# Kernel optimization log

Hardware: AMD Instinct MI355X
Metric: run time of the kernel (lower is better)

## Reference

```python
import jax, jax.numpy as jnp
import numpy as np

NEG_SLOPE = 0.2


def _gat_conv(x, src, dst, W, a_src, a_dst, b, n_nodes):
    # Single-head PyG GATConv (normalize arg in source is ignored by GATConv).
    h = x @ W                                   # [N, C_out]
    e_src = h @ a_src                           # [N] alpha_src contribution
    e_dst = h @ a_dst                           # [N] alpha_dst contribution
    logits = jax.nn.leaky_relu(e_src[src] + e_dst[dst], NEG_SLOPE)  # [E]
    m = jax.ops.segment_max(logits, dst, num_segments=n_nodes)      # per-dst max
    e = jnp.exp(logits - m[dst])
    denom = jax.ops.segment_sum(e, dst, num_segments=n_nodes)
    alpha = e / denom[dst]                      # edge softmax over in-neighbors
    out = jax.ops.segment_sum(h[src] * alpha[:, None], dst, num_segments=n_nodes)
    return out + b


def _add_self_loops(edge_index, n_nodes):
    loop = jnp.arange(n_nodes, dtype=edge_index.dtype)
    src = jnp.concatenate([edge_index[0], loop])
    dst = jnp.concatenate([edge_index[1], loop])
    return src, dst


def setup_inputs() -> dict:
    key = jax.random.key(0)
    ks = jax.random.split(key, 16)
    N, E, C_IN, C_HID, C_OUT = 50000, 1600000, 128, 128, 64
    x = jax.random.normal(ks[0], (N, C_IN), dtype=jnp.float32)
    edge_index = jax.random.randint(ks[1], (2, E), 0, N, dtype=jnp.int32)
    glorot = lambda k, shape: jax.random.normal(k, shape, jnp.float32) * np.sqrt(2.0 / sum(shape))
    return {
        "x": x,
        "edge_index": edge_index,
        "W0": glorot(ks[2], (C_IN, C_HID)),
        "as0": glorot(ks[3], (C_HID,)) * 0.1,
        "ad0": glorot(ks[4], (C_HID,)) * 0.1,
        "b0": jnp.zeros((C_HID,), jnp.float32),
        "W1": glorot(ks[5], (C_HID, C_HID)),
        "as1": glorot(ks[6], (C_HID,)) * 0.1,
        "ad1": glorot(ks[7], (C_HID,)) * 0.1,
        "b1": jnp.zeros((C_HID,), jnp.float32),
        "W2": glorot(ks[8], (C_HID, C_OUT)),
        "as2": glorot(ks[9], (C_OUT,)) * 0.1,
        "ad2": glorot(ks[10], (C_OUT,)) * 0.1,
        "b2": jnp.zeros((C_OUT,), jnp.float32),
    }


def reference(x, edge_index, W0, as0, ad0, b0, W1, as1, ad1, b1, W2, as2, ad2, b2):
    n_nodes = x.shape[0]
    src, dst = _add_self_loops(edge_index, n_nodes)
    # eval mode: F.dropout with training=False is identity
    h = jax.nn.relu(_gat_conv(x, src, dst, W0, as0, ad0, b0, n_nodes))
    h = jax.nn.relu(_gat_conv(h, src, dst, W1, as1, ad1, b1, n_nodes))
    out = _gat_conv(h, src, dst, W2, as2, ad2, b2, n_nodes)
    return out
```

## Files before the change

kernel.cpp:

```cpp
#include <hip/hip_runtime.h>
#include <hip/hip_bf16.h>
#include <type_traits>

#define DEVFN __device__ __forceinline__

typedef __attribute__((ext_vector_type(8))) short bfrag;
typedef __attribute__((ext_vector_type(4))) float facc4;
typedef __attribute__((ext_vector_type(2))) float f32x2;

DEVFN float lrelu(float v) { return (v >= 0.f) ? v : 0.2f * v; }

DEVFN float bf_lo(unsigned u) { return __uint_as_float(u << 16); }
DEVFN float bf_hi(unsigned u) { return __uint_as_float(u & 0xFFFF0000u); }
DEVFN f32x2 upk2(unsigned u) {
  f32x2 r; r.x = bf_lo(u); r.y = bf_hi(u); return r;
}
DEVFN unsigned short f2bf(float f) {
  __hip_bfloat16 h = __float2bfloat16(f);
  return *reinterpret_cast<unsigned short*>(&h);
}
DEVFN unsigned packbf2(float x, float y) {
  return (unsigned)f2bf(x) | ((unsigned)f2bf(y) << 16);
}

DEVFN float wave_sum(float v) {
#pragma unroll
  for (int o = 1; o < 64; o <<= 1) v += __shfl_xor(v, o, 64);
  return v;
}
DEVFN float wave_max(float v) {
#pragma unroll
  for (int o = 1; o < 64; o <<= 1) v = fmaxf(v, __shfl_xor(v, o, 64));
  return v;
}

#define FMA_ROW(p_, v_)                                                  \
  {                                                                      \
    f32x2 pv; pv.x = (p_); pv.y = (p_);                                  \
    acc2[0] += pv * upk2((v_).x);                                        \
    acc2[1] += pv * upk2((v_).y);                                        \
    acc2[2] += pv * upk2((v_).z);                                        \
    acc2[3] += pv * upk2((v_).w);                                        \
  }

template<int C, bool A_FP32>
__global__ __launch_bounds__(256) void gemm_mfma(const void* __restrict__ Xin,
                                                 const float* __restrict__ W,
                                                 const float* __restrict__ a_src,
                                                 const float* __restrict__ a_dst,
                                                 unsigned short* __restrict__ H,
                                                 float* __restrict__ es,
                                                 float* __restrict__ ed,
                                                 int N) {
  constexpr int K = 128;
  constexpr int LSTR = K + 8;
  constexpr int NT = C / 16;
  __shared__ unsigned short WsT[C * LSTR];

  const int t = threadIdx.x;
  for (int i = t; i < K * C; i += 256) {
    int k = i / C;
    int c = i - k * C;
    WsT[c * LSTR + k] = f2bf(W[i]);
  }
  __syncthreads();

  const int wave = t >> 6;
  const int lane = t & 63;
  const int l15 = lane & 15;
  const int quad = lane >> 4;
  const int arow = blockIdx.x * 64 + wave * 16 + l15;
  const bool avalid = arow < N;

  facc4 acc[NT];
#pragma unroll
  for (int i = 0; i < NT; ++i) acc[i] = (facc4){0.f, 0.f, 0.f, 0.f};

#pragma unroll
  for (int ks = 0; ks < 4; ++ks) {
    bfrag a;
    if (A_FP32) {
      if (avalid) {
        const float* xp = (const float*)Xin + (size_t)arow * K + quad * 8 + ks * 32;
        float4 u = *(const float4*)xp;
        float4 v = *(const float4*)(xp + 4);
        a[0] = (short)f2bf(u.x); a[1] = (short)f2bf(u.y);
        a[2] = (short)f2bf(u.z); a[3] = (short)f2bf(u.w);
        a[4] = (short)f2bf(v.x); a[5] = (short)f2bf(v.y);
        a[6] = (short)f2bf(v.z); a[7] = (short)f2bf(v.w);
      } else {
        a = (bfrag){0, 0, 0, 0, 0, 0, 0, 0};
      }
    } else {
      const unsigned short* xp =
          (const unsigned short*)Xin + (size_t)arow * K + quad * 8 + ks * 32;
      a = *(const bfrag*)xp;
    }
#pragma unroll
    for (int ct = 0; ct < NT; ++ct) {
      bfrag b = *(const bfrag*)(&WsT[(ct * 16 + l15) * LSTR + ks * 32 + quad * 8]);
      acc[ct] = __builtin_amdgcn_mfma_f32_16x16x32_bf16(a, b, acc[ct], 0, 0, 0);
    }
  }

  float asv[NT], adv[NT];
#pragma unroll
  for (int ct = 0; ct < NT; ++ct) {
    asv[ct] = a_src[ct * 16 + l15];
    adv[ct] = a_dst[ct * 16 + l15];
  }

  const int orow0 = blockIdx.x * 64 + wave * 16 + quad * 4;
#pragma unroll
  for (int r = 0; r < 4; ++r) {
    const int orow = orow0 + r;
    float ps = 0.f, pd = 0.f;
#pragma unroll
    for (int ct = 0; ct < NT; ++ct) {
      if (orow < N) H[(size_t)orow * C + ct * 16 + l15] = f2bf(acc[ct][r]);
      ps += acc[ct][r] * asv[ct];
      pd += acc[ct][r] * adv[ct];
    }
#pragma unroll
    for (int msk = 1; msk < 16; msk <<= 1) {
      ps += __shfl_xor(ps, msk, 64);
      pd += __shfl_xor(pd, msk, 64);
    }
    if (l15 == 0 && orow < N) { es[orow] = ps; ed[orow] = pd; }
  }
}

__global__ void hist_only(const int* __restrict__ dst, int* __restrict__ hmat,
                          int E, int nbk, int chunk) {
  __shared__ int hist[4 * 128];
  const int t = threadIdx.x;
  for (int i = t; i < 4 * 128; i += 256) hist[i] = 0;
  __syncthreads();
  int* h = &hist[(t >> 6) << 7];
  const int e0 = blockIdx.x * chunk;
  const int e1 = min(E, e0 + chunk);
  for (int e = e0 + t; e < e1; e += 256) {
    atomicAdd(&h[dst[e] >> 9], 1);
  }
  __syncthreads();
  if (t < nbk)
    hmat[t * gridDim.x + blockIdx.x] =
        hist[t] + hist[t + 128] + hist[t + 256] + hist[t + 384];
}

__global__ void scan_partial(const int* __restrict__ in, int* __restrict__ csum, int n) {
  __shared__ int sh[256];
  int i = blockIdx.x * 256 + threadIdx.x;
  sh[threadIdx.x] = (i < n) ? in[i] : 0;
  __syncthreads();
  for (int o = 128; o > 0; o >>= 1) {
    if (threadIdx.x < o) sh[threadIdx.x] += sh[threadIdx.x + o];
    __syncthreads();
  }
  if (threadIdx.x == 0) csum[blockIdx.x] = sh[0];
}

__global__ void scan_chunks(int* __restrict__ csum, int nch) {
  __shared__ int sh[256];
  __shared__ int carry;
  if (threadIdx.x == 0) carry = 0;
  __syncthreads();
  for (int base = 0; base < nch; base += 256) {
    int i = base + threadIdx.x;
    int v = (i < nch) ? csum[i] : 0;
    sh[threadIdx.x] = v;
    __syncthreads();
    for (int o = 1; o < 256; o <<= 1) {
      int t = (threadIdx.x >= o) ? sh[threadIdx.x - o] : 0;
      __syncthreads();
      sh[threadIdx.x] += t;
      __syncthreads();
    }
    if (i < nch) csum[i] = carry + sh[threadIdx.x] - v;
    __syncthreads();
    if (threadIdx.x == 255) carry += sh[255];
    __syncthreads();
  }
}

__global__ void scan_final(const int* __restrict__ deg, const int* __restrict__ csum,
                           int* __restrict__ rp, int* __restrict__ wp, int N, int E) {
  __shared__ int sh[256];
  int i = blockIdx.x * 256 + threadIdx.x;
  int v = (i < N) ? deg[i] : 0;
  sh[threadIdx.x] = v;
  __syncthreads();
  for (int o = 1; o < 256; o <<= 1) {
    int t = (threadIdx.x >= o) ? sh[threadIdx.x - o] : 0;
    __syncthreads();
    sh[threadIdx.x] += t;
    __syncthreads();
  }
  if (i < N) {
    int r = csum[blockIdx.x] + sh[threadIdx.x] - v;
    rp[i] = r;
    wp[i] = r;
  }
  if (blockIdx.x == 0 && threadIdx.x == 0) rp[N] = E;
}

__global__ void scan_final_excl(const int* __restrict__ in, const int* __restrict__ csum,
                                int* __restrict__ out, int n) {
  __shared__ int sh[256];
  int i = blockIdx.x * 256 + threadIdx.x;
  int v = (i < n) ? in[i] : 0;
  sh[threadIdx.x] = v;
  __syncthreads();
  for (int o = 1; o < 256; o <<= 1) {
    int t = (threadIdx.x >= o) ? sh[threadIdx.x - o] : 0;
    __syncthreads();
    sh[threadIdx.x] += t;
    __syncthreads();
  }
  if (i < n) out[i] = csum[blockIdx.x] + sh[threadIdx.x] - v;
}

__global__ void place_pass(const int* __restrict__ src, const int* __restrict__ dst,
                           const int* __restrict__ off, unsigned* __restrict__ be,
                           int E, int nbk, int chunk) {
  __shared__ int cur[128];
  const int t = threadIdx.x;
  if (t < nbk) cur[t] = off[t * gridDim.x + blockIdx.x];
  __syncthreads();
  const int e0 = blockIdx.x * chunk;
  const int e1 = min(E, e0 + chunk);
  for (int e = e0 + t; e < e1; e += 256) {
    int d = dst[e];
    int s = src[e];
    int p = atomicAdd(&cur[d >> 9], 1);
    be[p] = (unsigned)s | ((unsigned)d << 16);
  }
}

__global__ void bucket_final(const unsigned* __restrict__ be, const int* __restrict__ off,
                             int* __restrict__ rp, unsigned short* __restrict__ col,
                             int E, int N, int nbk, int pblk) {
  __shared__ int cur[512];
  __shared__ int ps[256];
  const int b = blockIdx.x;
  const int n0 = b << 9;
  const int cnt = min(512, N - n0);
  const int t = threadIdx.x;
  for (int i = t; i < cnt; i += 256) cur[i] = 0;
  __syncthreads();
  const int e0 = off[b * pblk];
  const int e1 = (b + 1 < nbk) ? off[(b + 1) * pblk] : E;
  for (int e = e0 + t; e < e1; e += 256) {
    unsigned sd = be[e];
    atomicAdd(&cur[(int)(sd >> 16) - n0], 1);
  }
  __syncthreads();
  const int i0 = 2 * t, i1 = 2 * t + 1;
  const int v0 = (i0 < cnt) ? cur[i0] : 0;
  const int v1 = (i1 < cnt) ? cur[i1] : 0;
  ps[t] = v0 + v1;
  __syncthreads();
  for (int o = 1; o < 256; o <<= 1) {
    int u = (t >= o) ? ps[t - o] : 0;
    __syncthreads();
    ps[t] += u;
    __syncthreads();
  }
  const int base = e0 + ps[t] - (v0 + v1);
  if (i0 < cnt) { rp[n0 + i0] = base;      cur[i0] = base; }
  if (i1 < cnt) { rp[n0 + i1] = base + v0; cur[i1] = base + v0; }
  if (b == nbk - 1 && t == 0) rp[N] = E;
  __syncthreads();
  for (int e = e0 + t; e < e1; e += 256) {
    unsigned sd = be[e];
    int p = atomicAdd(&cur[(int)(sd >> 16) - n0], 1);
    col[p] = (unsigned short)(sd & 0xFFFFu);
  }
}

__global__ void csr_scatter_ranged(const int* __restrict__ src,
                                   const int* __restrict__ dst,
                                   int* __restrict__ wp, int* __restrict__ col,
                                   int E, int range, int npass) {
  const int stride = gridDim.x * blockDim.x;
  const int gid = blockIdx.x * blockDim.x + threadIdx.x;
  for (int pass = 0; pass < npass; ++pass) {
    const int lo = pass * range;
    const int hi = lo + range;
    for (int e = gid; e < E; e += stride) {
      int d = dst[e];
      if (d >= lo && d < hi) {
        int p = atomicAdd(wp + d, 1);
        col[p] = src[e];
      }
    }
  }
}

__global__ void csr_count(const int* __restrict__ dst, int* __restrict__ deg, int E) {
  int e = blockIdx.x * blockDim.x + threadIdx.x;
  if (e < E) atomicAdd(deg + dst[e], 1);
}

template<bool RELU, typename IT>
__global__ void gat_fused128(const int* __restrict__ row_ptr,
                             const IT* __restrict__ col,
                             const float* __restrict__ es,
                             const float* __restrict__ ed,
                             const unsigned short* __restrict__ H,
                             const float* __restrict__ bias,
                             void* __restrict__ outX, int N) {
  const int lane = threadIdx.x & 63;
  const int n = blockIdx.x * (blockDim.x >> 6) + (threadIdx.x >> 6);
  if (n >= N) return;

  const int g4 = lane >> 4;
  const int l15 = lane & 15;

  const int k0 = row_ptr[n];
  const int k1 = row_ptr[n + 1];
  const int deg = k1 - k0;
  const float edd = ed[n];
  const float self_lg = lrelu(es[n] + edd);

  const char* Hb = (const char*)H;
  f32x2 acc2[4];
#pragma unroll
  for (int i = 0; i < 4; ++i) { acc2[i].x = 0.f; acc2[i].y = 0.f; }
  float den, sp;

  if (deg <= 64) {
    int k = k0 + lane;
    bool act = (k < k1);
    int c = act ? (int)col[k] : 0;
    float lg = act ? lrelu(es[c] + edd) : -3.0e38f;
    float m = fmaxf(wave_max(lg), self_lg);
    float p = act ? __expf(lg - m) : 0.f;
    sp = __expf(self_lg - m);
    den = wave_sum(p) + sp;

    if (deg > 0) {
      int i0 = g4;
      int i1 = min(4 + g4, 63);
      int c0 = __shfl(c, i0);
      int c1 = __shfl(c, i1);
      uint4 v0 = *(const uint4*)(Hb + (((size_t)c0 << 8) + l15 * 16));
      uint4 v1 = *(const uint4*)(Hb + (((size_t)c1 << 8) + l15 * 16));
      const int nb = (deg + 7) >> 3;
      for (int t = 0; t + 1 < nb; ++t) {
        int ni0 = min(8 * t + 8 + g4, 63);
        int ni1 = min(8 * t + 12 + g4, 63);
        int nc0 = __shfl(c, ni0);
        int nc1 = __shfl(c, ni1);
        uint4 u0 = *(const uint4*)(Hb + (((size_t)nc0 << 8) + l15 * 16));
        uint4 u1 = *(const uint4*)(Hb + (((size_t)nc1 << 8) + l15 * 16));
        float p0 = __shfl(p, i0);
        float p1 = __shfl(p, i1);
        FMA_ROW(p0, v0);
        FMA_ROW(p1, v1);
        v0 = u0; v1 = u1; i0 = ni0; i1 = ni1;
      }
      float p0 = __shfl(p, i0);
      float p1 = __shfl(p, i1);
      FMA_ROW(p0, v0);
      FMA_ROW(p1, v1);
    }
  } else {
    float mloc = self_lg;
    for (int base = k0; base < k1; base += 64) {
      int k = base + lane;
      if (k < k1) mloc = fmaxf(mloc, lrelu(es[(int)col[k]] + edd));
    }
    float m = wave_max(mloc);
    sp = __expf(self_lg - m);
    den = sp;
    for (int base = k0; base < k1; base += 64) {
      int k = base + lane;
      bool act = (k < k1);
      int c = act ? (int)col[k] : 0;
      float p = act ? __expf(lrelu(es[c] + edd) - m) : 0.f;
      den += wave_sum(p);
      int len = min(64, k1 - base);
      for (int j = 0; j < len; j += 8) {
        int i0 = min(j + g4, 63);
        int i1 = min(j + 4 + g4, 63);
        int c0 = __shfl(c, i0);
        int c1 = __shfl(c, i1);
        float p0 = __shfl(p, i0);
        float p1 = __shfl(p, i1);
        uint4 v0 = *(const uint4*)(Hb + (((size_t)c0 << 8) + l15 * 16));
        uint4 v1 = *(const uint4*)(Hb + (((size_t)c1 << 8) + l15 * 16));
        FMA_ROW(p0, v0);
        FMA_ROW(p1, v1);
      }
    }
  }

  float a[8];
#pragma unroll
  for (int i = 0; i < 4; ++i) { a[2 * i] = acc2[i].x; a[2 * i + 1] = acc2[i].y; }
#pragma unroll
  for (int i = 0; i < 8; ++i) {
    a[i] += __shfl_xor(a[i], 16, 64);
    a[i] += __shfl_xor(a[i], 32, 64);
  }

  uint4 hv = *(const uint4*)(Hb + (((size_t)n << 8) + l15 * 16));
  a[0] += sp * bf_lo(hv.x); a[1] += sp * bf_hi(hv.x);
  a[2] += sp * bf_lo(hv.y); a[3] += sp * bf_hi(hv.y);
  a[4] += sp * bf_lo(hv.z); a[5] += sp * bf_hi(hv.z);
  a[6] += sp * bf_lo(hv.w); a[7] += sp * bf_hi(hv.w);

  float inv = 1.f / den;
  float4 bv0 = *(const float4*)(bias + l15 * 8);
  float4 bv1 = *(const float4*)(bias + l15 * 8 + 4);
  float o0 = a[0] * inv + bv0.x, o1 = a[1] * inv + bv0.y;
  float o2 = a[2] * inv + bv0.z, o3 = a[3] * inv + bv0.w;
  float o4 = a[4] * inv + bv1.x, o5 = a[5] * inv + bv1.y;
  float o6 = a[6] * inv + bv1.z, o7 = a[7] * inv + bv1.w;
  if (RELU) {
    o0 = fmaxf(o0, 0.f); o1 = fmaxf(o1, 0.f); o2 = fmaxf(o2, 0.f);
    o3 = fmaxf(o3, 0.f); o4 = fmaxf(o4, 0.f); o5 = fmaxf(o5, 0.f);
    o6 = fmaxf(o6, 0.f); o7 = fmaxf(o7, 0.f);
  }
  if (g4 == 0) {
    uint4 w;
    w.x = packbf2(o0, o1); w.y = packbf2(o2, o3);
    w.z = packbf2(o4, o5); w.w = packbf2(o6, o7);
    *(uint4*)((char*)outX + (((size_t)n << 8) + l15 * 16)) = w;
  }
}

template<bool RELU, typename IT>
__global__ void gat_fused64(const int* __restrict__ row_ptr,
                            const IT* __restrict__ col,
                            const float* __restrict__ es,
                            const float* __restrict__ ed,
                            const unsigned short* __restrict__ H,
                            const float* __restrict__ bias,
                            float* __restrict__ outX, int N) {
  const int lane = threadIdx.x & 63;
  const int n = blockIdx.x * (blockDim.x >> 6) + (threadIdx.x >> 6);
  if (n >= N) return;

  const int g8 = lane >> 3;
  const int l8 = lane & 7;

  const int k0 = row_ptr[n];
  const int k1 = row_ptr[n + 1];
  const int deg = k1 - k0;
  const float edd = ed[n];
  const float self_lg = lrelu(es[n] + edd);

  const char* Hb = (const char*)H;
  f32x2 acc2[4];
#pragma unroll
  for (int i = 0; i < 4; ++i) { acc2[i].x = 0.f; acc2[i].y = 0.f; }
  float den, sp;

  if (deg <= 64) {
    int k = k0 + lane;
    bool act = (k < k1);
    int c = act ? (int)col[k] : 0;
    float lg = act ? lrelu(es[c] + edd) : -3.0e38f;
    float m = fmaxf(wave_max(lg), self_lg);
    float p = act ? __expf(lg - m) : 0.f;
    sp = __expf(self_lg - m);
    den = wave_sum(p) + sp;

    if (deg > 0) {
      int i0 = min(g8, 63);
      int i1 = min(8 + g8, 63);
      int c0 = __shfl(c, i0);
      int c1 = __shfl(c, i1);
      uint4 v0 = *(const uint4*)(Hb + (((size_t)c0 << 7) + l8 * 16));
      uint4 v1 = *(const uint4*)(Hb + (((size_t)c1 << 7) + l8 * 16));
      const int nb = (deg + 7) >> 3;
      for (int t = 0; t + 2 < nb; ++t) {
        int ni = min(8 * t + 16 + g8, 63);
        int nc = __shfl(c, ni);
        uint4 u = *(const uint4*)(Hb + (((size_t)nc << 7) + l8 * 16));
        float p0 = __shfl(p, i0);
        FMA_ROW(p0, v0);
        v0 = v1; v1 = u; i0 = i1; i1 = ni;
      }
      float p0 = __shfl(p, i0);
      FMA_ROW(p0, v0);
      if (nb > 1) {
        float p1 = __shfl(p, i1);
        FMA_ROW(p1, v1);
      }
    }
  } else {
    float mloc = self_lg;
    for (int base = k0; base < k1; base += 64) {
      int k = base + lane;
      if (k < k1) mloc = fmaxf(mloc, lrelu(es[(int)col[k]] + edd));
    }
    float m = wave_max(mloc);
    sp = __expf(self_lg - m);
    den = sp;
    for (int base = k0; base < k1; base += 64) {
      int k = base + lane;
      bool act = (k < k1);
      int c = act ? (int)col[k] : 0;
      float p = act ? __expf(lrelu(es[c] + edd) - m) : 0.f;
      den += wave_sum(p);
      int len = min(64, k1 - base);
      for (int j = 0; j < len; j += 8) {
        int i0 = min(j + g8, 63);
        int c0 = __shfl(c, i0);
        float p0 = __shfl(p, i0);
        uint4 v0 = *(const uint4*)(Hb + (((size_t)c0 << 7) + l8 * 16));
        FMA_ROW(p0, v0);
      }
    }
  }

  float a[8];
#pragma unroll
  for (int i = 0; i < 4; ++i) { a[2 * i] = acc2[i].x; a[2 * i + 1] = acc2[i].y; }
#pragma unroll
  for (int i = 0; i < 8; ++i) {
    a[i] += __shfl_xor(a[i], 8, 64);
    a[i] += __shfl_xor(a[i], 16, 64);
    a[i] += __shfl_xor(a[i], 32, 64);
  }

  uint4 hv = *(const uint4*)(Hb + (((size_t)n << 7) + l8 * 16));
  a[0] += sp * bf_lo(hv.x); a[1] += sp * bf_hi(hv.x);
  a[2] += sp * bf_lo(hv.y); a[3] += sp * bf_hi(hv.y);
  a[4] += sp * bf_lo(hv.z); a[5] += sp * bf_hi(hv.z);
  a[6] += sp * bf_lo(hv.w); a[7] += sp * bf_hi(hv.w);

  float inv = 1.f / den;
  float4 bv0 = *(const float4*)(bias + l8 * 8);
  float4 bv1 = *(const float4*)(bias + l8 * 8 + 4);
  float4 w0, w1;
  w0.x = a[0] * inv + bv0.x; w0.y = a[1] * inv + bv0.y;
  w0.z = a[2] * inv + bv0.z; w0.w = a[3] * inv + bv0.w;
  w1.x = a[4] * inv + bv1.x; w1.y = a[5] * inv + bv1.y;
  w1.z = a[6] * inv + bv1.z; w1.w = a[7] * inv + bv1.w;
  if (RELU) {
    w0.x = fmaxf(w0.x, 0.f); w0.y = fmaxf(w0.y, 0.f);
    w0.z = fmaxf(w0.z, 0.f); w0.w = fmaxf(w0.w, 0.f);
    w1.x = fmaxf(w1.x, 0.f); w1.y = fmaxf(w1.y, 0.f);
    w1.z = fmaxf(w1.z, 0.f); w1.w = fmaxf(w1.w, 0.f);
  }
  if (g8 == 0) {
    char* op = (char*)outX + (((size_t)n << 8) + l8 * 32);
    *(float4*)op = w0;
    *(float4*)(op + 16) = w1;
  }
}


extern "C" void kernel_launch(void* const* d_in, const int* in_sizes, int n_in,
                              void* d_out, int out_size, void* d_ws, size_t ws_size,
                              hipStream_t stream) {
  const int C_HID = in_sizes[3];
  const int C_FIN = in_sizes[11];
  const int C_IN  = in_sizes[2] / C_HID;
  const int N     = in_sizes[0] / C_IN;
  const int E     = in_sizes[1] / 2;
  const int NPAD  = ((N + 63) / 64) * 64;

  const float* x = (const float*)d_in[0];
  const int* ei  = (const int*)d_in[1];
  const int* src = ei;
  const int* dst = ei + E;

  const float* W0  = (const float*)d_in[2];
  const float* as0 = (const float*)d_in[3];
  const float* ad0 = (const float*)d_in[4];
  const float* b0  = (const float*)d_in[5];
  const float* W1  = (const float*)d_in[6];
  const float* as1 = (const float*)d_in[7];
  const float* ad1 = (const float*)d_in[8];
  const float* b1  = (const float*)d_in[9];
  const float* W2  = (const float*)d_in[10];
  const float* as2 = (const float*)d_in[11];
  const float* ad2 = (const float*)d_in[12];
  const float* b2  = (const float*)d_in[13];

  char* base = (char*)d_ws;
  size_t off = 0;
  auto alloc = [&](size_t bytes) -> char* {
    char* p = base + off;
    off = (off + bytes + 255) & ~((size_t)255);
    return p;
  };
  const int PBLK = 512;
  const int NBK  = (N + 511) >> 9;
  const int M    = NBK * PBLK;
  const int NCH  = (N + 255) / 256;
  const int MCH  = (M + 255) / 256;
  const int SCH  = (NCH > MCH ? NCH : MCH);

  unsigned short* XB  = (unsigned short*)alloc((size_t)NPAD * C_HID * 2);
  unsigned short* H   = (unsigned short*)alloc((size_t)N * C_HID * 2);
  float* ES    = (float*)alloc((size_t)N * sizeof(float));
  float* ED    = (float*)alloc((size_t)N * sizeof(float));
  int*   RP    = (int*)alloc((size_t)(N + 1) * sizeof(int));
  int*   WP    = (int*)alloc((size_t)N * sizeof(int));
  void*  COL   = (void*)alloc((size_t)E * sizeof(int));
  int*   DEG   = (int*)alloc((size_t)N * sizeof(int));
  int*   CSUM  = (int*)alloc((size_t)SCH * sizeof(int));
  int*   HMAT  = (int*)alloc((size_t)M * sizeof(int));
  int*   OFF   = (int*)alloc((size_t)M * sizeof(int));
  unsigned* BE = (unsigned*)alloc((size_t)E * sizeof(unsigned));
  (void)ws_size;

  const int wgrid = (N + 3) / 4;
  const int mgrid = NPAD / 64;
  const bool u16 = (N <= 65535);

  if (u16) {
    const int CHUNK = (E + PBLK - 1) / PBLK;
    hist_only<<<PBLK, 256, 0, stream>>>(dst, HMAT, E, NBK, CHUNK);
    scan_partial<<<MCH, 256, 0, stream>>>(HMAT, CSUM, M);
    scan_chunks<<<1, 256, 0, stream>>>(CSUM, MCH);
    scan_final_excl<<<MCH, 256, 0, stream>>>(HMAT, CSUM, OFF, M);
    place_pass<<<PBLK, 256, 0, stream>>>(src, dst, OFF, BE, E, NBK, CHUNK);
    bucket_final<<<NBK, 256, 0, stream>>>(BE, OFF, RP, (unsigned short*)COL,
                                          E, N, NBK, PBLK);
  } else {
    hipMemsetAsync(DEG, 0, (size_t)N * sizeof(int), stream);
    const int ET256 = (E + 255) / 256;
    csr_count<<<ET256, 256, 0, stream>>>(dst, DEG, E);
    scan_partial<<<NCH, 256, 0, stream>>>(DEG, CSUM, N);
    scan_chunks<<<1, 256, 0, stream>>>(CSUM, NCH);
    scan_final<<<NCH, 256, 0, stream>>>(DEG, CSUM, RP, WP, N, E);
    const int NPASS = 8;
    const int range = (N + NPASS - 1) / NPASS;
    csr_scatter_ranged<<<2048, 256, 0, stream>>>(src, dst, WP, (int*)COL, E,
                                                 range, NPASS);
  }

  auto run_layers = [&](auto* col) {
    using IT = typename std::remove_pointer<decltype(col)>::type;
    gemm_mfma<128, true><<<mgrid, 256, 0, stream>>>(x, W0, as0, ad0, H, ES, ED, N);
    gat_fused128<true, IT><<<wgrid, 256, 0, stream>>>(RP, col, ES, ED, H, b0, XB, N);
    gemm_mfma<128, false><<<mgrid, 256, 0, stream>>>(XB, W1, as1, ad1, H, ES, ED, N);
    gat_fused128<true, IT><<<wgrid, 256, 0, stream>>>(RP, col, ES, ED, H, b1, XB, N);
    gemm_mfma<64, false><<<mgrid, 256, 0, stream>>>(XB, W2, as2, ad2, H, ES, ED, N);
    gat_fused64<false, IT><<<wgrid, 256, 0, stream>>>(RP, col, ES, ED, H, b2,
                                                      (float*)d_out, N);
  };

  if (u16) run_layers((unsigned short*)COL);
  else     run_layers((int*)COL);
  (void)out_size; (void)n_in;
}
```

Before: 334.8 us.

## Split 128-wide GAT aggregation into two 64-column halves with cached softmax weights

The GEMM now writes the 128-channel feature matrix as two separate 64-column arrays. Each 128-wide attention aggregation becomes two kernels: the first computes softmax weights, stores them per edge along with the inverse denominator and self-loop weight, and aggregates the first half. The second reuses those stored weights to aggregate the second half. The intent is to halve the gathered working set per pass so it fits better in cache, at the cost of an extra launch, a second pass over the edge lists and extra per-edge weight traffic. It also drops the software prefetch in the gather loops and replaces the three-kernel offset scan with a single-block 1024-thread scan.

```diff
diff --git a/kernel.cpp b/kernel.cpp
--- a/kernel.cpp
+++ b/kernel.cpp
@@ -43,12 +43,13 @@
     acc2[3] += pv * upk2((v_).w);                                        \
   }
 
-template<int C, bool A_FP32>
+template<int C, bool A_FP32, bool SPLIT>
 __global__ __launch_bounds__(256) void gemm_mfma(const void* __restrict__ Xin,
                                                  const float* __restrict__ W,
                                                  const float* __restrict__ a_src,
                                                  const float* __restrict__ a_dst,
-                                                 unsigned short* __restrict__ H,
+                                                 unsigned short* __restrict__ H0,
+                                                 unsigned short* __restrict__ H1,
                                                  float* __restrict__ es,
                                                  float* __restrict__ ed,
                                                  int N) {
@@ -117,7 +118,14 @@
     float ps = 0.f, pd = 0.f;
 #pragma unroll
     for (int ct = 0; ct < NT; ++ct) {
-      if (orow < N) H[(size_t)orow * C + ct * 16 + l15] = f2bf(acc[ct][r]);
+      if (orow < N) {
+        if (SPLIT) {
+          unsigned short* Hh = (ct >= 4) ? H1 : H0;
+          Hh[(size_t)orow * 64 + (ct & 3) * 16 + l15] = f2bf(acc[ct][r]);
+        } else {
+          H0[(size_t)orow * C + ct * 16 + l15] = f2bf(acc[ct][r]);
+        }
+      }
       ps += acc[ct][r] * asv[ct];
       pd += acc[ct][r] * adv[ct];
     }
@@ -146,6 +154,26 @@
   if (t < nbk)
     hmat[t * gridDim.x + blockIdx.x] =
         hist[t] + hist[t + 128] + hist[t + 256] + hist[t + 384];
+}
+
+__global__ void scan_all(const int* __restrict__ in, int* __restrict__ out, int n) {
+  __shared__ int sh[1024];
+  const int t = threadIdx.x;
+  const int per = (n + 1023) >> 10;
+  const int b0 = t * per;
+  const int b1 = min(b0 + per, n);
+  int s = 0;
+  for (int i = b0; i < b1; ++i) s += in[i];
+  sh[t] = s;
+  __syncthreads();
+  for (int o = 1; o < 1024; o <<= 1) {
+    int u = (t >= o) ? sh[t - o] : 0;
+    __syncthreads();
+    sh[t] += u;
+    __syncthreads();
+  }
+  int ex = sh[t] - s;
+  for (int i = b0; i < b1; ++i) { int v = in[i]; out[i] = ex; ex += v; }
 }
 
 __global__ void scan_partial(const int* __restrict__ in, int* __restrict__ csum, int n) {
@@ -202,22 +230,6 @@
     wp[i] = r;
   }
   if (blockIdx.x == 0 && threadIdx.x == 0) rp[N] = E;
-}
-
-__global__ void scan_final_excl(const int* __restrict__ in, const int* __restrict__ csum,
-                                int* __restrict__ out, int n) {
-  __shared__ int sh[256];
-  int i = blockIdx.x * 256 + threadIdx.x;
-  int v = (i < n) ? in[i] : 0;
-  sh[threadIdx.x] = v;
-  __syncthreads();
-  for (int o = 1; o < 256; o <<= 1) {
-    int t = (threadIdx.x >= o) ? sh[threadIdx.x - o] : 0;
-    __syncthreads();
-    sh[threadIdx.x] += t;
-    __syncthreads();
-  }
-  if (i < n) out[i] = csum[blockIdx.x] + sh[threadIdx.x] - v;
 }
 
 __global__ void place_pass(const int* __restrict__ src, const int* __restrict__ dst,
@@ -303,19 +315,22 @@
 }
 
 template<bool RELU, typename IT>
-__global__ void gat_fused128(const int* __restrict__ row_ptr,
-                             const IT* __restrict__ col,
-                             const float* __restrict__ es,
-                             const float* __restrict__ ed,
-                             const unsigned short* __restrict__ H,
-                             const float* __restrict__ bias,
-                             void* __restrict__ outX, int N) {
+__global__ void gat_half_a(const int* __restrict__ row_ptr,
+                           const IT* __restrict__ col,
+                           const float* __restrict__ es,
+                           const float* __restrict__ ed,
+                           const unsigned short* __restrict__ H0,
+                           const float* __restrict__ bias,
+                           float* __restrict__ P,
+                           float* __restrict__ DENI,
+                           float* __restrict__ SPV,
+                           unsigned short* __restrict__ XB, int N) {
   const int lane = threadIdx.x & 63;
   const int n = blockIdx.x * (blockDim.x >> 6) + (threadIdx.x >> 6);
   if (n >= N) return;
 
-  const int g4 = lane >> 4;
-  const int l15 = lane & 15;
+  const int g8 = lane >> 3;
+  const int l8 = lane & 7;
 
   const int k0 = row_ptr[n];
   const int k1 = row_ptr[n + 1];
@@ -323,7 +338,7 @@
   const float edd = ed[n];
   const float self_lg = lrelu(es[n] + edd);
 
-  const char* Hb = (const char*)H;
+  const char* Hb = (const char*)H0;
   f32x2 acc2[4];
 #pragma unroll
   for (int i = 0; i < 4; ++i) { acc2[i].x = 0.f; acc2[i].y = 0.f; }
@@ -338,32 +353,13 @@
     float p = act ? __expf(lg - m) : 0.f;
     sp = __expf(self_lg - m);
     den = wave_sum(p) + sp;
-
-    if (deg > 0) {
-      int i0 = g4;
-      int i1 = min(4 + g4, 63);
+    if (act) P[k] = p;
+    for (int j = 0; j < deg; j += 8) {
+      int i0 = min(j + g8, 63);
       int c0 = __shfl(c, i0);
-      int c1 = __shfl(c, i1);
-      uint4 v0 = *(const uint4*)(Hb + (((size_t)c0 << 8) + l15 * 16));
-      uint4 v1 = *(const uint4*)(Hb + (((size_t)c1 << 8) + l15 * 16));
-      const int nb = (deg + 7) >> 3;
-      for (int t = 0; t + 1 < nb; ++t) {
-        int ni0 = min(8 * t + 8 + g4, 63);
-        int ni1 = min(8 * t + 12 + g4, 63);
-        int nc0 = __shfl(c, ni0);
-        int nc1 = __shfl(c, ni1);
-        uint4 u0 = *(const uint4*)(Hb + (((size_t)nc0 << 8) + l15 * 16));
-        uint4 u1 = *(const uint4*)(Hb + (((size_t)nc1 << 8) + l15 * 16));
-        float p0 = __shfl(p, i0);
-        float p1 = __shfl(p, i1);
-        FMA_ROW(p0, v0);
-        FMA_ROW(p1, v1);
-        v0 = u0; v1 = u1; i0 = ni0; i1 = ni1;
-      }
       float p0 = __shfl(p, i0);
-      float p1 = __shfl(p, i1);
+      uint4 v0 = *(const uint4*)(Hb + (((size_t)c0 << 7) + l8 * 16));
       FMA_ROW(p0, v0);
-      FMA_ROW(p1, v1);
     }
   } else {
     float mloc = self_lg;
@@ -379,19 +375,15 @@
       bool act = (k < k1);
       int c = act ? (int)col[k] : 0;
       float p = act ? __expf(lrelu(es[c] + edd) - m) : 0.f;
+      if (act) P[k] = p;
       den += wave_sum(p);
       int len = min(64, k1 - base);
       for (int j = 0; j < len; j += 8) {
-        int i0 = min(j + g4, 63);
-        int i1 = min(j + 4 + g4, 63);
+        int i0 = min(j + g8, 63);
         int c0 = __shfl(c, i0);
-        int c1 = __shfl(c, i1);
         float p0 = __shfl(p, i0);
-        float p1 = __shfl(p, i1);
-        uint4 v0 = *(const uint4*)(Hb + (((size_t)c0 << 8) + l15 * 16));
-        uint4 v1 = *(const uint4*)(Hb + (((size_t)c1 << 8) + l15 * 16));
+        uint4 v0 = *(const uint4*)(Hb + (((size_t)c0 << 7) + l8 * 16));
         FMA_ROW(p0, v0);
-        FMA_ROW(p1, v1);
       }
     }
   }
@@ -401,19 +393,21 @@
   for (int i = 0; i < 4; ++i) { a[2 * i] = acc2[i].x; a[2 * i + 1] = acc2[i].y; }
 #pragma unroll
   for (int i = 0; i < 8; ++i) {
+    a[i] += __shfl_xor(a[i], 8, 64);
     a[i] += __shfl_xor(a[i], 16, 64);
     a[i] += __shfl_xor(a[i], 32, 64);
   }
 
-  uint4 hv = *(const uint4*)(Hb + (((size_t)n << 8) + l15 * 16));
+  uint4 hv = *(const uint4*)(Hb + (((size_t)n << 7) + l8 * 16));
   a[0] += sp * bf_lo(hv.x); a[1] += sp * bf_hi(hv.x);
   a[2] += sp * bf_lo(hv.y); a[3] += sp * bf_hi(hv.y);
   a[4] += sp * bf_lo(hv.z); a[5] += sp * bf_hi(hv.z);
   a[6] += sp * bf_lo(hv.w); a[7] += sp * bf_hi(hv.w);
 
   float inv = 1.f / den;
-  float4 bv0 = *(const float4*)(bias + l15 * 8);
-  float4 bv1 = *(const float4*)(bias + l15 * 8 + 4);
+  if (lane == 0) { DENI[n] = inv; SPV[n] = sp; }
+  float4 bv0 = *(const float4*)(bias + l8 * 8);
+  float4 bv1 = *(const float4*)(bias + l8 * 8 + 4);
   float o0 = a[0] * inv + bv0.x, o1 = a[1] * inv + bv0.y;
   float o2 = a[2] * inv + bv0.z, o3 = a[3] * inv + bv0.w;
   float o4 = a[4] * inv + bv1.x, o5 = a[5] * inv + bv1.y;
@@ -423,11 +417,102 @@
     o3 = fmaxf(o3, 0.f); o4 = fmaxf(o4, 0.f); o5 = fmaxf(o5, 0.f);
     o6 = fmaxf(o6, 0.f); o7 = fmaxf(o7, 0.f);
   }
-  if (g4 == 0) {
+  if (g8 == 0) {
     uint4 w;
     w.x = packbf2(o0, o1); w.y = packbf2(o2, o3);
     w.z = packbf2(o4, o5); w.w = packbf2(o6, o7);
-    *(uint4*)((char*)outX + (((size_t)n << 8) + l15 * 16)) = w;
+    *(uint4*)((char*)XB + (((size_t)n << 8) + l8 * 16)) = w;
+  }
+}
+
+template<bool RELU, typename IT>
+__global__ void gat_half_b(const int* __restrict__ row_ptr,
+                           const IT* __restrict__ col,
+                           const float* __restrict__ P,
+                           const float* __restrict__ DENI,
+                           const float* __restrict__ SPV,
+                           const unsigned short* __restrict__ H1,
+                           const float* __restrict__ bias,
+                           unsigned short* __restrict__ XB, int N) {
+  const int lane = threadIdx.x & 63;
+  const int n = blockIdx.x * (blockDim.x >> 6) + (threadIdx.x >> 6);
+  if (n >= N) return;
+
+  const int g8 = lane >> 3;
+  const int l8 = lane & 7;
+
+  const int k0 = row_ptr[n];
+  const int k1 = row_ptr[n + 1];
+  const int deg = k1 - k0;
+  const float sp = SPV[n];
+  const float inv = DENI[n];
+
+  const char* Hb = (const char*)H1;
+  f32x2 acc2[4];
+#pragma unroll
+  for (int i = 0; i < 4; ++i) { acc2[i].x = 0.f; acc2[i].y = 0.f; }
+
+  if (deg <= 64) {
+    int k = k0 + lane;
+    bool act = (k < k1);
+    int c = act ? (int)col[k] : 0;
+    float p = act ? P[k] : 0.f;
+    for (int j = 0; j < deg; j += 8) {
+      int i0 = min(j + g8, 63);
+      int c0 = __shfl(c, i0);
+      float p0 = __shfl(p, i0);
+      uint4 v0 = *(const uint4*)(Hb + (((size_t)c0 << 7) + l8 * 16));
+      FMA_ROW(p0, v0);
+    }
+  } else {
+    for (int base = k0; base < k1; base += 64) {
+      int k = base + lane;
+      bool act = (k < k1);
+      int c = act ? (int)col[k] : 0;
+      float p = act ? P[k] : 0.f;
+      int len = min(64, k1 - base);
+      for (int j = 0; j < len; j += 8) {
+        int i0 = min(j + g8, 63);
+        int c0 = __shfl(c, i0);
+        float p0 = __shfl(p, i0);
+        uint4 v0 = *(const uint4*)(Hb + (((size_t)c0 << 7) + l8 * 16));
+        FMA_ROW(p0, v0);
+      }
+    }
+  }
+
+  float a[8];
+#pragma unroll
+  for (int i = 0; i < 4; ++i) { a[2 * i] = acc2[i].x; a[2 * i + 1] = acc2[i].y; }
+#pragma unroll
+  for (int i = 0; i < 8; ++i) {
+    a[i] += __shfl_xor(a[i], 8, 64);
+    a[i] += __shfl_xor(a[i], 16, 64);
+    a[i] += __shfl_xor(a[i], 32, 64);
+  }
+
+  uint4 hv = *(const uint4*)(Hb + (((size_t)n << 7) + l8 * 16));
+  a[0] += sp * bf_lo(hv.x); a[1] += sp * bf_hi(hv.x);
+  a[2] += sp * bf_lo(hv.y); a[3] += sp * bf_hi(hv.y);
+  a[4] += sp * bf_lo(hv.z); a[5] += sp * bf_hi(hv.z);
+  a[6] += sp * bf_lo(hv.w); a[7] += sp * bf_hi(hv.w);
+
+  float4 bv0 = *(const float4*)(bias + 64 + l8 * 8);
+  float4 bv1 = *(const float4*)(bias + 64 + l8 * 8 + 4);
+  float o0 = a[0] * inv + bv0.x, o1 = a[1] * inv + bv0.y;
+  float o2 = a[2] * inv + bv0.z, o3 = a[3] * inv + bv0.w;
+  float o4 = a[4] * inv + bv1.x, o5 = a[5] * inv + bv1.y;
+  float o6 = a[6] * inv + bv1.z, o7 = a[7] * inv + bv1.w;
+  if (RELU) {
+    o0 = fmaxf(o0, 0.f); o1 = fmaxf(o1, 0.f); o2 = fmaxf(o2, 0.f);
+    o3 = fmaxf(o3, 0.f); o4 = fmaxf(o4, 0.f); o5 = fmaxf(o5, 0.f);
+    o6 = fmaxf(o6, 0.f); o7 = fmaxf(o7, 0.f);
+  }
+  if (g8 == 0) {
+    uint4 w;
+    w.x = packbf2(o0, o1); w.y = packbf2(o2, o3);
+    w.z = packbf2(o4, o5); w.w = packbf2(o6, o7);
+    *(uint4*)((char*)XB + (((size_t)n << 8) + 128 + l8 * 16)) = w;
   }
 }
 
@@ -467,29 +552,12 @@
     float p = act ? __expf(lg - m) : 0.f;
     sp = __expf(self_lg - m);
     den = wave_sum(p) + sp;
-
-    if (deg > 0) {
-      int i0 = min(g8, 63);
-      int i1 = min(8 + g8, 63);
+    for (int j = 0; j < deg; j += 8) {
+      int i0 = min(j + g8, 63);
       int c0 = __shfl(c, i0);
-      int c1 = __shfl(c, i1);
+      float p0 = __shfl(p, i0);
       uint4 v0 = *(const uint4*)(Hb + (((size_t)c0 << 7) + l8 * 16));
-      uint4 v1 = *(const uint4*)(Hb + (((size_t)c1 << 7) + l8 * 16));
-      const int nb = (deg + 7) >> 3;
-      for (int t = 0; t + 2 < nb; ++t) {
-        int ni = min(8 * t + 16 + g8, 63);
-        int nc = __shfl(c, ni);
-        uint4 u = *(const uint4*)(Hb + (((size_t)nc << 7) + l8 * 16));
-        float p0 = __shfl(p, i0);
-        FMA_ROW(p0, v0);
-        v0 = v1; v1 = u; i0 = i1; i1 = ni;
-      }
-      float p0 = __shfl(p, i0);
       FMA_ROW(p0, v0);
-      if (nb > 1) {
-        float p1 = __shfl(p, i1);
-        FMA_ROW(p1, v1);
-      }
     }
   } else {
     float mloc = self_lg;
@@ -594,13 +662,16 @@
   const int NBK  = (N + 511) >> 9;
   const int M    = NBK * PBLK;
   const int NCH  = (N + 255) / 256;
-  const int MCH  = (M + 255) / 256;
-  const int SCH  = (NCH > MCH ? NCH : MCH);
+  const int SCH  = NCH;
 
   unsigned short* XB  = (unsigned short*)alloc((size_t)NPAD * C_HID * 2);
-  unsigned short* H   = (unsigned short*)alloc((size_t)N * C_HID * 2);
+  unsigned short* H0  = (unsigned short*)alloc((size_t)N * 64 * 2);
+  unsigned short* H1  = (unsigned short*)alloc((size_t)N * 64 * 2);
   float* ES    = (float*)alloc((size_t)N * sizeof(float));
   float* ED    = (float*)alloc((size_t)N * sizeof(float));
+  float* P     = (float*)alloc((size_t)E * sizeof(float));
+  float* DENI  = (float*)alloc((size_t)N * sizeof(float));
+  float* SPV   = (float*)alloc((size_t)N * sizeof(float));
   int*   RP    = (int*)alloc((size_t)(N + 1) * sizeof(int));
   int*   WP    = (int*)alloc((size_t)N * sizeof(int));
   void*  COL   = (void*)alloc((size_t)E * sizeof(int));
@@ -618,9 +689,7 @@
   if (u16) {
     const int CHUNK = (E + PBLK - 1) / PBLK;
     hist_only<<<PBLK, 256, 0, stream>>>(dst, HMAT, E, NBK, CHUNK);
-    scan_partial<<<MCH, 256, 0, stream>>>(HMAT, CSUM, M);
-    scan_chunks<<<1, 256, 0, stream>>>(CSUM, MCH);
-    scan_final_excl<<<MCH, 256, 0, stream>>>(HMAT, CSUM, OFF, M);
+    scan_all<<<1, 1024, 0, stream>>>(HMAT, OFF, M);
     place_pass<<<PBLK, 256, 0, stream>>>(src, dst, OFF, BE, E, NBK, CHUNK);
     bucket_final<<<NBK, 256, 0, stream>>>(BE, OFF, RP, (unsigned short*)COL,
                                           E, N, NBK, PBLK);
@@ -639,12 +708,21 @@
 
   auto run_layers = [&](auto* col) {
     using IT = typename std::remove_pointer<decltype(col)>::type;
-    gemm_mfma<128, true><<<mgrid, 256, 0, stream>>>(x, W0, as0, ad0, H, ES, ED, N);
-    gat_fused128<true, IT><<<wgrid, 256, 0, stream>>>(RP, col, ES, ED, H, b0, XB, N);
-    gemm_mfma<128, false><<<mgrid, 256, 0, stream>>>(XB, W1, as1, ad1, H, ES, ED, N);
-    gat_fused128<true, IT><<<wgrid, 256, 0, stream>>>(RP, col, ES, ED, H, b1, XB, N);
-    gemm_mfma<64, false><<<mgrid, 256, 0, stream>>>(XB, W2, as2, ad2, H, ES, ED, N);
-    gat_fused64<false, IT><<<wgrid, 256, 0, stream>>>(RP, col, ES, ED, H, b2,
+    gemm_mfma<128, true, true><<<mgrid, 256, 0, stream>>>(x, W0, as0, ad0,
+                                                          H0, H1, ES, ED, N);
+    gat_half_a<true, IT><<<wgrid, 256, 0, stream>>>(RP, col, ES, ED, H0, b0,
+                                                    P, DENI, SPV, XB, N);
+    gat_half_b<true, IT><<<wgrid, 256, 0, stream>>>(RP, col, P, DENI, SPV,
+                                                    H1, b0, XB, N);
+    gemm_mfma<128, false, true><<<mgrid, 256, 0, stream>>>(XB, W1, as1, ad1,
+                                                           H0, H1, ES, ED, N);
+    gat_half_a<true, IT><<<wgrid, 256, 0, stream>>>(RP, col, ES, ED, H0, b1,
+                                                    P, DENI, SPV, XB, N);
+    gat_half_b<true, IT><<<wgrid, 256, 0, stream>>>(RP, col, P, DENI, SPV,
+                                                    H1, b1, XB, N);
+    gemm_mfma<64, false, false><<<mgrid, 256, 0, stream>>>(XB, W2, as2, ad2,
+                                                           H0, H1, ES, ED, N);
+    gat_fused64<false, IT><<<wgrid, 256, 0, stream>>>(RP, col, ES, ED, H0, b2,
                                                       (float*)d_out, N);
   };
 
```

Result: slower. 434.2 us (+29.7%).
